# Optimization experiments

Hardware: AMD Instinct MI355X
Metric: run time of the kernel (lower is better)

The kernel has to match this reference:

```python
import jax, jax.numpy as jnp
import numpy as np

B, S, D_MODEL, D_SPACE = 4, 2048, 1024, 64
N = 512            # size of each neuron pool (all six equal)
TOTAL = 6 * N      # neuron_emb rows
K = 8              # top_k for all four attention branches
EPS = 1e-8


def topk_sparsify(w, k):
    """Top-k sparsification with renormalization via dense one-hot scatter-sum.
    w: [..., N] softmax probs -> sparse renormalized [..., N]."""
    vals, idx = jax.lax.top_k(w, k)                       # [..., k]
    n = w.shape[-1]
    one_hot = jax.nn.one_hot(idx, n, dtype=w.dtype)       # [..., k, N]
    sparse = (one_hot * vals[..., None]).sum(axis=-2)     # [..., N]
    return sparse / (sparse.sum(axis=-1, keepdims=True) + EPS)


def setup_inputs() -> dict:
    key = jax.random.key(0)
    kx, kw, ke = jax.random.split(key, 3)
    x = jax.random.normal(kx, (B, S, D_MODEL), dtype=jnp.float32)
    W_all = jax.random.normal(kw, (D_MODEL, 6 * D_SPACE), dtype=jnp.float32) * 0.02
    b_all = jnp.zeros((6 * D_SPACE,), dtype=jnp.float32)
    neuron_emb = jax.random.normal(ke, (TOTAL, D_SPACE), dtype=jnp.float32) * 0.02
    return {"x": x, "W_all": W_all, "b_all": b_all, "neuron_emb": neuron_emb}


def reference(x, W_all, b_all, neuron_emb):
    # L2-normalized neuron embeddings (cosine-sim logits)
    emb = neuron_emb / (jnp.linalg.norm(neuron_emb, axis=-1, keepdims=True) + EPS)
    # dense projection, then split into 6 heads of d_space (deterministic: no dropout)
    proj = x @ W_all + b_all                              # [B,S,6*d_space]
    h = jnp.split(proj, 6, axis=-1)
    # neuron_emb segments: fqk, fv, rqk, rv (knowledge segments unused here)
    segs = [emb[0:N], emb[0:N], emb[N:2 * N], emb[2 * N:3 * N], emb[2 * N:3 * N], emb[3 * N:4 * N]]
    weights = []
    for hi, ei in zip(h, segs):
        logits = jnp.einsum('bsd,nd->bsn', hi, ei)        # [B,S,N]
        pref = jax.nn.softmax(logits, axis=-1)
        weights.append(topk_sparsify(pref, K))
    # [6, B, S, N]: (fqk_Q, fqk_K, fv, rqk_Q, rqk_K, rv)
    return jnp.stack(weights, axis=0)
```

## Files before the change

### kernel.cpp

```cpp
#include <hip/hip_runtime.h>
#include <math.h>

#define NB 4
#define NS 2048
#define DMODEL 1024
#define DSPACE 64
#define NPOOL 512
#define NHEADS 6
#define NTOK (NB * NS)
#define PROJN (NHEADS * DSPACE)
#define EPSF 1e-8f

typedef float f32x2 __attribute__((ext_vector_type(2)));

#define PK_LO(ACC, A2, B2) \
    asm("v_pk_fma_f32 %0, %1, %2, %0 op_sel:[0,0,0] op_sel_hi:[1,0,1]" \
        : "+v"(ACC) : "v"(A2), "v"(B2))
#define PK_HI(ACC, A2, B2) \
    asm("v_pk_fma_f32 %0, %1, %2, %0 op_sel:[0,1,0] op_sel_hi:[1,1,1]" \
        : "+v"(ACC) : "v"(A2), "v"(B2))

__global__ __launch_bounds__(256) void k_norm_emb(const float* __restrict__ emb,
                                                  float* __restrict__ embT) {
    int row  = blockIdx.x * 4 + (threadIdx.x >> 6);
    int lane = threadIdx.x & 63;
    float v  = emb[row * DSPACE + lane];
    float ss = v * v;
#pragma unroll
    for (int off = 32; off >= 1; off >>= 1) ss += __shfl_xor(ss, off, 64);
    float nrm = sqrtf(ss) + EPSF;
    embT[lane * 2048 + row] = v / nrm;
}

__global__ __launch_bounds__(128, 4) void k_proj(const float* __restrict__ X,
                                                 const float* __restrict__ W,
                                                 const float* __restrict__ bias,
                                                 float* __restrict__ P, int KS) {
    __shared__ float Xt[2][16 * 128];
    __shared__ float Wt[2][16 * 64];
    const int tid = threadIdx.x;
    const int bm  = blockIdx.x * 128;
    const int bn  = blockIdx.y * 64;
    const int z   = blockIdx.z;
    float* Pp = P + (size_t)z * NTOK * PROJN;

    const int r0  = (tid >> 3) << 2;
    const int c0  = (tid & 7) << 2;
    const int lwr = tid >> 3;
    const int lwc = (tid & 7) << 3;

    const float* Xrow = X + (size_t)(bm + tid) * DMODEL;

    f32x2 acc2[4][8];
#pragma unroll
    for (int p = 0; p < 4; ++p)
#pragma unroll
        for (int j = 0; j < 8; ++j) acc2[p][j] = (f32x2){0.f, 0.f};

    const int nsteps = KS >> 4;
    int k0 = z * KS;
    float4 xr0 = *(const float4*)&Xrow[k0 + 0];
    float4 xr1 = *(const float4*)&Xrow[k0 + 4];
    float4 xr2 = *(const float4*)&Xrow[k0 + 8];
    float4 xr3 = *(const float4*)&Xrow[k0 + 12];
    float4 wg0 = *(const float4*)&W[(size_t)(k0 + lwr) * PROJN + bn + lwc];
    float4 wg1 = *(const float4*)&W[(size_t)(k0 + lwr) * PROJN + bn + lwc + 4];

    {
        float* xb = Xt[0]; float* wb = Wt[0];
        xb[ 0*128+tid]=xr0.x; xb[ 1*128+tid]=xr0.y; xb[ 2*128+tid]=xr0.z; xb[ 3*128+tid]=xr0.w;
        xb[ 4*128+tid]=xr1.x; xb[ 5*128+tid]=xr1.y; xb[ 6*128+tid]=xr1.z; xb[ 7*128+tid]=xr1.w;
        xb[ 8*128+tid]=xr2.x; xb[ 9*128+tid]=xr2.y; xb[10*128+tid]=xr2.z; xb[11*128+tid]=xr2.w;
        xb[12*128+tid]=xr3.x; xb[13*128+tid]=xr3.y; xb[14*128+tid]=xr3.z; xb[15*128+tid]=xr3.w;
        *(float4*)&wb[lwr * 64 + lwc]     = wg0;
        *(float4*)&wb[lwr * 64 + lwc + 4] = wg1;
    }

    for (int s = 0; s < nsteps; ++s) {
        if (s + 1 < nsteps) {
            int k1 = k0 + 16;
            xr0 = *(const float4*)&Xrow[k1 + 0];
            xr1 = *(const float4*)&Xrow[k1 + 4];
            xr2 = *(const float4*)&Xrow[k1 + 8];
            xr3 = *(const float4*)&Xrow[k1 + 12];
            wg0 = *(const float4*)&W[(size_t)(k1 + lwr) * PROJN + bn + lwc];
            wg1 = *(const float4*)&W[(size_t)(k1 + lwr) * PROJN + bn + lwc + 4];
        }
        __syncthreads();
        if (s + 1 < nsteps) {
            float* xb = Xt[(s + 1) & 1]; float* wb = Wt[(s + 1) & 1];
            xb[ 0*128+tid]=xr0.x; xb[ 1*128+tid]=xr0.y; xb[ 2*128+tid]=xr0.z; xb[ 3*128+tid]=xr0.w;
            xb[ 4*128+tid]=xr1.x; xb[ 5*128+tid]=xr1.y; xb[ 6*128+tid]=xr1.z; xb[ 7*128+tid]=xr1.w;
            xb[ 8*128+tid]=xr2.x; xb[ 9*128+tid]=xr2.y; xb[10*128+tid]=xr2.z; xb[11*128+tid]=xr2.w;
            xb[12*128+tid]=xr3.x; xb[13*128+tid]=xr3.y; xb[14*128+tid]=xr3.z; xb[15*128+tid]=xr3.w;
            *(float4*)&wb[lwr * 64 + lwc]     = wg0;
            *(float4*)&wb[lwr * 64 + lwc + 4] = wg1;
        }
        const float* xc = Xt[s & 1];
        const float* wc = Wt[s & 1];
#pragma unroll
        for (int kk = 0; kk < 16; ++kk) {
            float4 a0 = *(const float4*)&xc[kk * 128 + r0];
            float4 a1 = *(const float4*)&xc[kk * 128 + r0 + 64];
            float4 b0 = *(const float4*)&wc[kk * 64 + c0];
            float4 b1 = *(const float4*)&wc[kk * 64 + c0 + 32];
            f32x2 ap0 = (f32x2){a0.x, a0.y};
            f32x2 ap1 = (f32x2){a0.z, a0.w};
            f32x2 ap2 = (f32x2){a1.x, a1.y};
            f32x2 ap3 = (f32x2){a1.z, a1.w};
            f32x2 bq0 = (f32x2){b0.x, b0.y};
            f32x2 bq1 = (f32x2){b0.z, b0.w};
            f32x2 bq2 = (f32x2){b1.x, b1.y};
            f32x2 bq3 = (f32x2){b1.z, b1.w};
#pragma unroll
            for (int p = 0; p < 4; ++p) {
                f32x2 ap = (p == 0) ? ap0 : (p == 1) ? ap1 : (p == 2) ? ap2 : ap3;
                PK_LO(acc2[p][0], ap, bq0); PK_HI(acc2[p][1], ap, bq0);
                PK_LO(acc2[p][2], ap, bq1); PK_HI(acc2[p][3], ap, bq1);
                PK_LO(acc2[p][4], ap, bq2); PK_HI(acc2[p][5], ap, bq2);
                PK_LO(acc2[p][6], ap, bq3); PK_HI(acc2[p][7], ap, bq3);
            }
        }
        k0 += 16;
    }

#pragma unroll
    for (int i = 0; i < 8; ++i) {
        int row = bm + r0 + ((i < 4) ? i : 60 + i);
        float o0[4], o1[4];
#pragma unroll
        for (int j = 0; j < 4; ++j) {
            f32x2 v0 = acc2[i >> 1][j];
            f32x2 v1 = acc2[i >> 1][j + 4];
            o0[j] = (i & 1) ? v0.y : v0.x;
            o1[j] = (i & 1) ? v1.y : v1.x;
        }
        if (z == 0) {
#pragma unroll
            for (int j = 0; j < 4; ++j) {
                o0[j] += bias[bn + c0 + j];
                o1[j] += bias[bn + c0 + 32 + j];
            }
        }
        *(float4*)&Pp[(size_t)row * PROJN + bn + c0]      = *(float4*)&o0[0];
        *(float4*)&Pp[(size_t)row * PROJN + bn + c0 + 32] = *(float4*)&o1[0];
    }
}

#define CE(arr, a, b) { float _hi = fmaxf(arr[a], arr[b]); arr[b] = fminf(arr[a], arr[b]); arr[a] = _hi; }

#define SORT8(s) \
    CE(s,0,1) CE(s,2,3) CE(s,4,5) CE(s,6,7) \
    CE(s,0,2) CE(s,1,3) CE(s,4,6) CE(s,5,7) \
    CE(s,1,2) CE(s,5,6) \
    CE(s,0,4) CE(s,1,5) CE(s,2,6) CE(s,3,7) \
    CE(s,2,4) CE(s,3,5) \
    CE(s,1,2) CE(s,3,4) CE(s,5,6)

#define SWZ(v, IMM) __int_as_float(__builtin_amdgcn_ds_swizzle(__float_as_int(v), IMM))

#define BFLY_LEVEL(XCHG) { \
    float q[4][8]; \
    _Pragma("unroll") \
    for (int tt = 0; tt < 4; ++tt) { \
        _Pragma("unroll") \
        for (int i = 0; i < 8; ++i) { float _x = s[tt][i]; q[tt][i] = XCHG(_x); } \
    } \
    _Pragma("unroll") \
    for (int tt = 0; tt < 4; ++tt) { \
        float c[8]; \
        c[0] = fmaxf(s[tt][0], q[tt][7]); c[1] = fmaxf(s[tt][1], q[tt][6]); \
        c[2] = fmaxf(s[tt][2], q[tt][5]); c[3] = fmaxf(s[tt][3], q[tt][4]); \
        c[4] = fmaxf(s[tt][4], q[tt][3]); c[5] = fmaxf(s[tt][5], q[tt][2]); \
        c[6] = fmaxf(s[tt][6], q[tt][1]); c[7] = fmaxf(s[tt][7], q[tt][0]); \
        CE(c,0,4) CE(c,1,5) CE(c,2,6) CE(c,3,7) \
        CE(c,0,2) CE(c,1,3) CE(c,4,6) CE(c,5,7) \
        CE(c,0,1) CE(c,2,3) CE(c,4,5) CE(c,6,7) \
        _Pragma("unroll") \
        for (int i = 0; i < 8; ++i) s[tt][i] = c[i]; \
    } }

#define X1(v)  SWZ(v, 0x041F)
#define X2(v)  SWZ(v, 0x081F)
#define X4_(v) SWZ(v, 0x101F)
#define X8(v)  SWZ(v, 0x201F)
#define X16(v) SWZ(v, 0x401F)
#define X32(v) __shfl_xor(v, 32, 64)

__global__ __launch_bounds__(128, 4) void k_router(const float* __restrict__ P,
                                                   const float* __restrict__ embT,
                                                   float* __restrict__ out, int SK) {
    __shared__ float hsh[16][DSPACE];
    const int head = blockIdx.y;
    const int t0   = blockIdx.x * 16;
    const int tid  = threadIdx.x;
    const int wid  = tid >> 6;
    const int lane = tid & 63;
    const int so = (head == 2) ? 512 : (head == 3 || head == 4) ? 1024
                 : (head == 5) ? 1536 : 0;

    {
        int t  = (wid << 3) + (lane >> 3);
        int d0 = (lane & 7) << 3;
        size_t off = (size_t)(t0 + t) * PROJN + head * DSPACE + d0;
        float4 v0 = *(const float4*)&P[off];
        float4 v1 = *(const float4*)&P[off + 4];
        for (int ks = 1; ks < SK; ++ks) {
            size_t o2 = (size_t)ks * NTOK * PROJN + off;
            float4 u0 = *(const float4*)&P[o2];
            float4 u1 = *(const float4*)&P[o2 + 4];
            v0.x += u0.x; v0.y += u0.y; v0.z += u0.z; v0.w += u0.w;
            v1.x += u1.x; v1.y += u1.y; v1.z += u1.z; v1.w += u1.w;
        }
        *(float4*)&hsh[t][d0]     = v0;
        *(float4*)&hsh[t][d0 + 4] = v1;
    }

    f32x2 acc2[8][4];
#pragma unroll
    for (int t = 0; t < 8; ++t)
#pragma unroll
        for (int p = 0; p < 4; ++p) acc2[t][p] = (f32x2){0.f, 0.f};

    const float* ebase = &embT[so + (lane << 3)];
    for (int d4 = 0; d4 < DSPACE; d4 += 4) {
        f32x2 hp[8][2];
#pragma unroll
        for (int t = 0; t < 8; ++t) {
            hp[t][0] = *(const f32x2*)&hsh[(wid << 3) + t][d4];
            hp[t][1] = *(const f32x2*)&hsh[(wid << 3) + t][d4 + 2];
        }
#pragma unroll
        for (int dp = 0; dp < 2; ++dp) {
            const float* er0 = ebase + (size_t)(d4 + 2 * dp) * 2048;
            const float* er1 = er0 + 2048;
            f32x2 ea[4], eb[4];
#pragma unroll
            for (int p = 0; p < 4; ++p) {
                ea[p] = *(const f32x2*)&er0[2 * p];
                eb[p] = *(const f32x2*)&er1[2 * p];
            }
#pragma unroll
            for (int t = 0; t < 8; ++t) {
#pragma unroll
                for (int p = 0; p < 4; ++p) {
                    PK_LO(acc2[t][p], ea[p], hp[t][dp]);
                    PK_HI(acc2[t][p], eb[p], hp[t][dp]);
                }
            }
        }
    }

    const size_t obase = ((size_t)head * NTOK + t0 + (wid << 3)) * NPOOL;

#pragma unroll
    for (int g = 0; g < 2; ++g) {
        float l[4][8], s[4][8];
#pragma unroll
        for (int tt = 0; tt < 4; ++tt)
#pragma unroll
            for (int j = 0; j < 8; ++j) {
                f32x2 v = acc2[4 * g + tt][j >> 1];
                l[tt][j] = (j & 1) ? v.y : v.x;
                s[tt][j] = l[tt][j];
            }

        SORT8(s[0]) SORT8(s[1]) SORT8(s[2]) SORT8(s[3])

        BFLY_LEVEL(X1)
        BFLY_LEVEL(X2)
        BFLY_LEVEL(X4_)
        BFLY_LEVEL(X8)
        BFLY_LEVEL(X16)
        BFLY_LEVEL(X32)

        unsigned gtm[4], eqm[4]; int own[4], inc[4];
#pragma unroll
        for (int tt = 0; tt < 4; ++tt) {
            const float T = s[tt][7];
            unsigned g_ = 0, e_ = 0; int cg = 0, ce = 0;
#pragma unroll
            for (int j = 0; j < 8; ++j) {
                if (l[tt][j] > T)       { g_ |= 1u << j; ++cg; }
                else if (l[tt][j] == T) { e_ |= 1u << j; ++ce; }
            }
            gtm[tt] = g_; eqm[tt] = e_;
            own[tt] = (ce << 8) | cg;
            inc[tt] = own[tt];
        }
#pragma unroll
        for (int off = 1; off < 64; off <<= 1) {
            int v0 = __shfl_up(inc[0], off, 64);
            int v1 = __shfl_up(inc[1], off, 64);
            int v2 = __shfl_up(inc[2], off, 64);
            int v3 = __shfl_up(inc[3], off, 64);
            if (lane >= off) { inc[0] += v0; inc[1] += v1; inc[2] += v2; inc[3] += v3; }
        }

#pragma unroll
        for (int tt = 0; tt < 4; ++tt) {
            const float T = s[tt][7];
            const float m = s[tt][0];
            int tot  = __shfl(inc[tt], 63, 64);
            int need = 8 - (tot & 0xff);
            int eqpre = (inc[tt] - own[tt]) >> 8;
            unsigned sel = gtm[tt];
#pragma unroll
            for (int j = 0; j < 8; ++j) {
                if ((eqm[tt] >> j) & 1u) { if (eqpre < need) sel |= 1u << j; ++eqpre; }
            }

            float s8 = 0.f;
#pragma unroll
            for (int i = 0; i < 8; ++i) s8 += __expf(s[tt][i] - m);
            float invd = 1.0f / s8;

            float o[8];
#pragma unroll
            for (int j = 0; j < 8; ++j)
                o[j] = ((sel >> j) & 1u) ? __expf(l[tt][j] - m) * invd : 0.0f;
            float4* dst = (float4*)&out[obase + (size_t)(4 * g + tt) * NPOOL + (lane << 3)];
            dst[0] = *(float4*)&o[0];
            dst[1] = *(float4*)&o[4];
        }
    }
}

extern "C" void kernel_launch(void* const* d_in, const int* in_sizes, int n_in,
                              void* d_out, int out_size, void* d_ws, size_t ws_size,
                              hipStream_t stream) {
    const float* x   = (const float*)d_in[0];
    const float* W   = (const float*)d_in[1];
    const float* b   = (const float*)d_in[2];
    const float* emb = (const float*)d_in[3];
    float* out  = (float*)d_out;
    float* embT = (float*)d_ws;
    float* proj = embT + 64 * 2048;

    size_t base = (size_t)64 * 2048 * 4;
    size_t slab = (size_t)NTOK * PROJN * 4;
    int SK = (ws_size >= base + 4 * slab) ? 4
           : (ws_size >= base + 2 * slab) ? 2 : 1;
    int KS = DMODEL / SK;

    k_norm_emb<<<dim3(512), dim3(256), 0, stream>>>(emb, embT);
    dim3 g2(NTOK / 128, PROJN / 64, SK);
    k_proj<<<g2, dim3(128), 0, stream>>>(x, W, b, proj, KS);
    dim3 g3(NTOK / 16, NHEADS);
    k_router<<<g3, dim3(128), 0, stream>>>(proj, embT, out, SK);
}
```

Before: 183.8 us.

## Split router tokens across four waves with per-token top-k processing

The router block grows from 2 to 4 waves, each owning 4 tokens instead of 8. The top-k butterfly merge and prefix-scan selection now handle one token at a time rather than four interleaved, which lowers register pressure and allows a higher occupancy target in the launch bounds. In exchange, each wave reuses every embedding load across fewer tokens, so embedding traffic from L2 doubles. The serial shuffle chains also lose the instruction-level parallelism that interleaving four tokens gave.

```diff
diff --git a/kernel.cpp b/kernel.cpp
--- a/kernel.cpp
+++ b/kernel.cpp
@@ -159,26 +159,20 @@
 
 #define SWZ(v, IMM) __int_as_float(__builtin_amdgcn_ds_swizzle(__float_as_int(v), IMM))
 
-#define BFLY_LEVEL(XCHG) { \
-    float q[4][8]; \
+#define BFLY1(s, XCHG) { \
+    float q[8]; \
     _Pragma("unroll") \
-    for (int tt = 0; tt < 4; ++tt) { \
-        _Pragma("unroll") \
-        for (int i = 0; i < 8; ++i) { float _x = s[tt][i]; q[tt][i] = XCHG(_x); } \
-    } \
+    for (int i = 0; i < 8; ++i) { float _x = s[i]; q[i] = XCHG(_x); } \
+    float c[8]; \
+    c[0] = fmaxf(s[0], q[7]); c[1] = fmaxf(s[1], q[6]); \
+    c[2] = fmaxf(s[2], q[5]); c[3] = fmaxf(s[3], q[4]); \
+    c[4] = fmaxf(s[4], q[3]); c[5] = fmaxf(s[5], q[2]); \
+    c[6] = fmaxf(s[6], q[1]); c[7] = fmaxf(s[7], q[0]); \
+    CE(c,0,4) CE(c,1,5) CE(c,2,6) CE(c,3,7) \
+    CE(c,0,2) CE(c,1,3) CE(c,4,6) CE(c,5,7) \
+    CE(c,0,1) CE(c,2,3) CE(c,4,5) CE(c,6,7) \
     _Pragma("unroll") \
-    for (int tt = 0; tt < 4; ++tt) { \
-        float c[8]; \
-        c[0] = fmaxf(s[tt][0], q[tt][7]); c[1] = fmaxf(s[tt][1], q[tt][6]); \
-        c[2] = fmaxf(s[tt][2], q[tt][5]); c[3] = fmaxf(s[tt][3], q[tt][4]); \
-        c[4] = fmaxf(s[tt][4], q[tt][3]); c[5] = fmaxf(s[tt][5], q[tt][2]); \
-        c[6] = fmaxf(s[tt][6], q[tt][1]); c[7] = fmaxf(s[tt][7], q[tt][0]); \
-        CE(c,0,4) CE(c,1,5) CE(c,2,6) CE(c,3,7) \
-        CE(c,0,2) CE(c,1,3) CE(c,4,6) CE(c,5,7) \
-        CE(c,0,1) CE(c,2,3) CE(c,4,5) CE(c,6,7) \
-        _Pragma("unroll") \
-        for (int i = 0; i < 8; ++i) s[tt][i] = c[i]; \
-    } }
+    for (int i = 0; i < 8; ++i) s[i] = c[i]; }
 
 #define X1(v)  SWZ(v, 0x041F)
 #define X2(v)  SWZ(v, 0x081F)
@@ -187,7 +181,7 @@
 #define X16(v) SWZ(v, 0x401F)
 #define X32(v) __shfl_xor(v, 32, 64)
 
-__global__ __launch_bounds__(128, 4) void k_router(const float* __restrict__ P,
+__global__ __launch_bounds__(256, 8) void k_router(const float* __restrict__ P,
                                                    const float* __restrict__ embT,
                                                    float* __restrict__ out, int SK) {
     __shared__ float hsh[16][DSPACE];
@@ -200,129 +194,105 @@
                  : (head == 5) ? 1536 : 0;
 
     {
-        int t  = (wid << 3) + (lane >> 3);
-        int d0 = (lane & 7) << 3;
+        int t  = (wid << 2) + (lane >> 4);
+        int d0 = (lane & 15) << 2;
         size_t off = (size_t)(t0 + t) * PROJN + head * DSPACE + d0;
         float4 v0 = *(const float4*)&P[off];
-        float4 v1 = *(const float4*)&P[off + 4];
         for (int ks = 1; ks < SK; ++ks) {
-            size_t o2 = (size_t)ks * NTOK * PROJN + off;
-            float4 u0 = *(const float4*)&P[o2];
-            float4 u1 = *(const float4*)&P[o2 + 4];
+            float4 u0 = *(const float4*)&P[(size_t)ks * NTOK * PROJN + off];
             v0.x += u0.x; v0.y += u0.y; v0.z += u0.z; v0.w += u0.w;
-            v1.x += u1.x; v1.y += u1.y; v1.z += u1.z; v1.w += u1.w;
-        }
-        *(float4*)&hsh[t][d0]     = v0;
-        *(float4*)&hsh[t][d0 + 4] = v1;
-    }
-
-    f32x2 acc2[8][4];
-#pragma unroll
-    for (int t = 0; t < 8; ++t)
+        }
+        *(float4*)&hsh[t][d0] = v0;
+    }
+
+    f32x2 acc2[4][4];
+#pragma unroll
+    for (int t = 0; t < 4; ++t)
 #pragma unroll
         for (int p = 0; p < 4; ++p) acc2[t][p] = (f32x2){0.f, 0.f};
 
     const float* ebase = &embT[so + (lane << 3)];
-    for (int d4 = 0; d4 < DSPACE; d4 += 4) {
-        f32x2 hp[8][2];
-#pragma unroll
-        for (int t = 0; t < 8; ++t) {
-            hp[t][0] = *(const f32x2*)&hsh[(wid << 3) + t][d4];
-            hp[t][1] = *(const f32x2*)&hsh[(wid << 3) + t][d4 + 2];
-        }
-#pragma unroll
-        for (int dp = 0; dp < 2; ++dp) {
-            const float* er0 = ebase + (size_t)(d4 + 2 * dp) * 2048;
-            const float* er1 = er0 + 2048;
-            f32x2 ea[4], eb[4];
+    for (int d2 = 0; d2 < DSPACE; d2 += 2) {
+        f32x2 hp[4];
+#pragma unroll
+        for (int t = 0; t < 4; ++t)
+            hp[t] = *(const f32x2*)&hsh[(wid << 2) + t][d2];
+        const float* er0 = ebase + (size_t)d2 * 2048;
+        const float* er1 = er0 + 2048;
+        f32x2 ea[4], eb[4];
+#pragma unroll
+        for (int p = 0; p < 4; ++p) {
+            ea[p] = *(const f32x2*)&er0[2 * p];
+            eb[p] = *(const f32x2*)&er1[2 * p];
+        }
+#pragma unroll
+        for (int t = 0; t < 4; ++t) {
 #pragma unroll
             for (int p = 0; p < 4; ++p) {
-                ea[p] = *(const f32x2*)&er0[2 * p];
-                eb[p] = *(const f32x2*)&er1[2 * p];
+                PK_LO(acc2[t][p], ea[p], hp[t]);
+                PK_HI(acc2[t][p], eb[p], hp[t]);
             }
-#pragma unroll
-            for (int t = 0; t < 8; ++t) {
-#pragma unroll
-                for (int p = 0; p < 4; ++p) {
-                    PK_LO(acc2[t][p], ea[p], hp[t][dp]);
-                    PK_HI(acc2[t][p], eb[p], hp[t][dp]);
-                }
-            }
-        }
-    }
-
-    const size_t obase = ((size_t)head * NTOK + t0 + (wid << 3)) * NPOOL;
-
-#pragma unroll
-    for (int g = 0; g < 2; ++g) {
-        float l[4][8], s[4][8];
-#pragma unroll
-        for (int tt = 0; tt < 4; ++tt)
-#pragma unroll
-            for (int j = 0; j < 8; ++j) {
-                f32x2 v = acc2[4 * g + tt][j >> 1];
-                l[tt][j] = (j & 1) ? v.y : v.x;
-                s[tt][j] = l[tt][j];
-            }
-
-        SORT8(s[0]) SORT8(s[1]) SORT8(s[2]) SORT8(s[3])
-
-        BFLY_LEVEL(X1)
-        BFLY_LEVEL(X2)
-        BFLY_LEVEL(X4_)
-        BFLY_LEVEL(X8)
-        BFLY_LEVEL(X16)
-        BFLY_LEVEL(X32)
-
-        unsigned gtm[4], eqm[4]; int own[4], inc[4];
-#pragma unroll
-        for (int tt = 0; tt < 4; ++tt) {
-            const float T = s[tt][7];
-            unsigned g_ = 0, e_ = 0; int cg = 0, ce = 0;
-#pragma unroll
-            for (int j = 0; j < 8; ++j) {
-                if (l[tt][j] > T)       { g_ |= 1u << j; ++cg; }
-                else if (l[tt][j] == T) { e_ |= 1u << j; ++ce; }
-            }
-            gtm[tt] = g_; eqm[tt] = e_;
-            own[tt] = (ce << 8) | cg;
-            inc[tt] = own[tt];
-        }
+        }
+    }
+
+    const size_t obase = ((size_t)head * NTOK + t0 + (wid << 2)) * NPOOL;
+
+#pragma unroll
+    for (int t = 0; t < 4; ++t) {
+        float l[8], s[8];
+#pragma unroll
+        for (int j = 0; j < 8; ++j) {
+            f32x2 v = acc2[t][j >> 1];
+            l[j] = (j & 1) ? v.y : v.x;
+            s[j] = l[j];
+        }
+
+        SORT8(s)
+
+        BFLY1(s, X1)
+        BFLY1(s, X2)
+        BFLY1(s, X4_)
+        BFLY1(s, X8)
+        BFLY1(s, X16)
+        BFLY1(s, X32)
+
+        const float T = s[7];
+        const float m = s[0];
+
+        unsigned gtm = 0, eqm = 0; int cgt = 0, ceq = 0;
+#pragma unroll
+        for (int j = 0; j < 8; ++j) {
+            if (l[j] > T)       { gtm |= 1u << j; ++cgt; }
+            else if (l[j] == T) { eqm |= 1u << j; ++ceq; }
+        }
+        int own = (ceq << 8) | cgt;
+        int inc = own;
 #pragma unroll
         for (int off = 1; off < 64; off <<= 1) {
-            int v0 = __shfl_up(inc[0], off, 64);
-            int v1 = __shfl_up(inc[1], off, 64);
-            int v2 = __shfl_up(inc[2], off, 64);
-            int v3 = __shfl_up(inc[3], off, 64);
-            if (lane >= off) { inc[0] += v0; inc[1] += v1; inc[2] += v2; inc[3] += v3; }
-        }
-
-#pragma unroll
-        for (int tt = 0; tt < 4; ++tt) {
-            const float T = s[tt][7];
-            const float m = s[tt][0];
-            int tot  = __shfl(inc[tt], 63, 64);
-            int need = 8 - (tot & 0xff);
-            int eqpre = (inc[tt] - own[tt]) >> 8;
-            unsigned sel = gtm[tt];
-#pragma unroll
-            for (int j = 0; j < 8; ++j) {
-                if ((eqm[tt] >> j) & 1u) { if (eqpre < need) sel |= 1u << j; ++eqpre; }
-            }
-
-            float s8 = 0.f;
-#pragma unroll
-            for (int i = 0; i < 8; ++i) s8 += __expf(s[tt][i] - m);
-            float invd = 1.0f / s8;
-
-            float o[8];
-#pragma unroll
-            for (int j = 0; j < 8; ++j)
-                o[j] = ((sel >> j) & 1u) ? __expf(l[tt][j] - m) * invd : 0.0f;
-            float4* dst = (float4*)&out[obase + (size_t)(4 * g + tt) * NPOOL + (lane << 3)];
-            dst[0] = *(float4*)&o[0];
-            dst[1] = *(float4*)&o[4];
-        }
+            int v = __shfl_up(inc, off, 64);
+            if (lane >= off) inc += v;
+        }
+        int tot  = __shfl(inc, 63, 64);
+        int need = 8 - (tot & 0xff);
+        int eqpre = (inc - own) >> 8;
+        unsigned sel = gtm;
+#pragma unroll
+        for (int j = 0; j < 8; ++j) {
+            if ((eqm >> j) & 1u) { if (eqpre < need) sel |= 1u << j; ++eqpre; }
+        }
+
+        float s8 = 0.f;
+#pragma unroll
+        for (int i = 0; i < 8; ++i) s8 += __expf(s[i] - m);
+        float invd = 1.0f / s8;
+
+        float o[8];
+#pragma unroll
+        for (int j = 0; j < 8; ++j)
+            o[j] = ((sel >> j) & 1u) ? __expf(l[j] - m) * invd : 0.0f;
+        float4* dst = (float4*)&out[obase + (size_t)t * NPOOL + (lane << 3)];
+        dst[0] = *(float4*)&o[0];
+        dst[1] = *(float4*)&o[4];
     }
 }
 
@@ -347,5 +317,5 @@
     dim3 g2(NTOK / 128, PROJN / 64, SK);
     k_proj<<<g2, dim3(128), 0, stream>>>(x, W, b, proj, KS);
     dim3 g3(NTOK / 16, NHEADS);
-    k_router<<<g3, dim3(128), 0, stream>>>(proj, embT, out, SK);
+    k_router<<<g3, dim3(256), 0, stream>>>(proj, embT, out, SK);
 }
```

After: 181.0 us. Within noise of the previous version (-1.5%).
